# Optimization experiments

Measured on AMD Instinct MI355X. Metric: run time of the kernel, lower is better.

The kernel has to match this reference:

```python
import jax, jax.numpy as jnp
import numpy as np
from jax import lax

B, C_IN, C_OUT, N, R, K = 16, 64, 64, 32768, 32, 3
GROUPS, GN_EPS = 8, 1e-5


def swish(x):
    return x * jax.nn.sigmoid(x)


def group_norm(x, gamma, beta):
    b, c = x.shape[:2]
    xg = x.reshape(b, GROUPS, -1)
    mu = xg.mean(-1, keepdims=True)
    var = xg.var(-1, keepdims=True)
    xn = ((xg - mu) * lax.rsqrt(var + GN_EPS)).reshape(x.shape)
    shp = (1, c) + (1,) * (x.ndim - 2)
    return xn * gamma.reshape(shp) + beta.reshape(shp)


def conv3d(x, w, b):
    y = lax.conv_general_dilated(x, w, (1, 1, 1), 'SAME',
                                 dimension_numbers=('NCDHW', 'OIDHW', 'NCDHW'))
    return y + b.reshape(1, -1, 1, 1, 1)


def voxelize(features, coords):
    # features [B,C,N], coords [B,3,N] -> vox [B,C,R,R,R], norm_coords [B,3,N] in [0,R-1]
    c = coords - coords.mean(axis=2, keepdims=True)
    scale = jnp.linalg.norm(c, axis=1, keepdims=True).max(axis=2, keepdims=True) * 2.0  # eps=0
    norm = jnp.clip((c / scale + 0.5) * R, 0.0, R - 1)
    vc = jnp.round(norm).astype(jnp.int32)
    idx = (vc[:, 0] * R + vc[:, 1]) * R + vc[:, 2]  # [B,N] flat voxel index

    def per_batch(f, i):  # f [C,N], i [N] -> [C, R^3] scatter-average
        sums = jax.ops.segment_sum(f.T, i, num_segments=R ** 3)  # [R^3, C]
        cnt = jax.ops.segment_sum(jnp.ones(i.shape, f.dtype), i, num_segments=R ** 3)
        return (sums / jnp.maximum(cnt, 1.0)[:, None]).T

    vox = jax.vmap(per_batch)(features, idx).reshape(features.shape[0], features.shape[1], R, R, R)
    return vox, norm


def trilinear_devoxelize(vox, coords):
    # vox [B,C,R,R,R], coords [B,3,N] float in [0,R-1] -> [B,C,N]
    b, c = vox.shape[:2]
    flat = vox.reshape(b, c, R ** 3)
    c0f = jnp.floor(coords)
    f = coords - c0f
    i0 = jnp.clip(c0f.astype(jnp.int32), 0, R - 1)
    i1 = jnp.clip(i0 + 1, 0, R - 1)
    out = jnp.zeros((b, c, coords.shape[2]), vox.dtype)
    for xi, wx in ((i0[:, 0], 1.0 - f[:, 0]), (i1[:, 0], f[:, 0])):
        for yi, wy in ((i0[:, 1], 1.0 - f[:, 1]), (i1[:, 1], f[:, 1])):
            for zi, wz in ((i0[:, 2], 1.0 - f[:, 2]), (i1[:, 2], f[:, 2])):
                idx = (xi * R + yi) * R + zi  # [B,N]
                w = (wx * wy * wz)[:, None, :]
                out = out + jnp.take_along_axis(flat, idx[:, None, :], axis=2) * w
    return out


def setup_inputs():
    key = jax.random.key(0)
    ks = jax.random.split(key, 6)
    s1 = 1.0 / np.sqrt(C_IN * K ** 3)
    s2 = 1.0 / np.sqrt(C_OUT * K ** 3)
    sp = 1.0 / np.sqrt(C_IN)
    return {
        'features': jax.random.normal(ks[0], (B, C_IN, N), jnp.float32),
        'coords': jax.random.normal(ks[1], (B, 3, N), jnp.float32),
        'w1': jax.random.normal(ks[2], (C_OUT, C_IN, K, K, K), jnp.float32) * s1,
        'b1': jnp.zeros((C_OUT,), jnp.float32),
        'g1': jnp.ones((C_OUT,), jnp.float32),
        'be1': jnp.zeros((C_OUT,), jnp.float32),
        'w2': jax.random.normal(ks[3], (C_OUT, C_OUT, K, K, K), jnp.float32) * s2,
        'b2': jnp.zeros((C_OUT,), jnp.float32),
        'g2': jnp.ones((C_OUT,), jnp.float32),
        'be2': jnp.zeros((C_OUT,), jnp.float32),
        'wp': jax.random.normal(ks[4], (C_OUT, C_IN), jnp.float32) * sp,
        'bp': jnp.zeros((C_OUT,), jnp.float32),
        'gp': jnp.ones((C_OUT,), jnp.float32),
        'bep': jnp.zeros((C_OUT,), jnp.float32),
    }


def reference(features, coords, w1, b1, g1, be1, w2, b2, g2, be2, wp, bp, gp, bep):
    coords_sg = lax.stop_gradient(coords)  # torch: coords.detach() inside Voxelization
    vox, norm_coords = voxelize(features, coords_sg)
    h = swish(group_norm(conv3d(vox, w1, b1), g1, be1))
    # Dropout(0.1) is identity in eval mode
    h = swish(group_norm(conv3d(h, w2, b2), g2, be2))
    vpts = trilinear_devoxelize(h, norm_coords)
    pf = swish(group_norm(jnp.einsum('oc,bcn->bon', wp, features) + bp[None, :, None], gp, bep))
    return (vpts + pf, coords)
```

## Files before the change

kernel.cpp:

```cpp
#include <hip/hip_runtime.h>
#include <hip/hip_bf16.h>
#include <math.h>

#define BB   16
#define CCH  64
#define NPT  32768
#define RR   32
#define R3   32768
#define GSZ  262144
#define VOXB 2228224

typedef __attribute__((ext_vector_type(8))) short bfx8;
typedef __attribute__((ext_vector_type(8))) unsigned short usx8;
typedef __attribute__((ext_vector_type(16))) float f32x16;

__device__ __forceinline__ short f2bf(float f) {
    unsigned u = __builtin_bit_cast(unsigned, f);
    u += 0x7fff + ((u >> 16) & 1);
    return (short)(u >> 16);
}
__device__ __forceinline__ float bf2f(unsigned short s) {
    unsigned u = ((unsigned)s) << 16;
    return __builtin_bit_cast(float, u);
}

__device__ __forceinline__ float blockReduceSumF(float v) {
    __shared__ float sm[16];
    #pragma unroll
    for (int o = 32; o > 0; o >>= 1) v += __shfl_down(v, o);
    __syncthreads();
    if ((threadIdx.x & 63) == 0) sm[threadIdx.x >> 6] = v;
    __syncthreads();
    float s = 0.f;
    int nw = blockDim.x >> 6;
    for (int i = 0; i < nw; ++i) s += sm[i];
    return s;
}

__device__ __forceinline__ float blockReduceMaxF(float v) {
    __shared__ float sm[16];
    #pragma unroll
    for (int o = 32; o > 0; o >>= 1) v = fmaxf(v, __shfl_down(v, o));
    __syncthreads();
    if ((threadIdx.x & 63) == 0) sm[threadIdx.x >> 6] = v;
    __syncthreads();
    float s = sm[0];
    int nw = blockDim.x >> 6;
    for (int i = 1; i < nw; ++i) s = fmaxf(s, sm[i]);
    return s;
}

__global__ void k_cstat_sum(const float* __restrict__ coords, float* __restrict__ csum) {
    int b = blockIdx.x >> 3, seg = blockIdx.x & 7;
    const float* cb = coords + (size_t)b * 3 * NPT;
    int n0 = seg << 12;
    float sx = 0.f, sy = 0.f, sz = 0.f;
    for (int n = n0 + threadIdx.x; n < n0 + 4096; n += 256) {
        sx += cb[n]; sy += cb[NPT + n]; sz += cb[2 * NPT + n];
    }
    sx = blockReduceSumF(sx);
    sy = blockReduceSumF(sy);
    sz = blockReduceSumF(sz);
    if (threadIdx.x == 0) {
        atomicAdd(&csum[b * 4 + 0], sx);
        atomicAdd(&csum[b * 4 + 1], sy);
        atomicAdd(&csum[b * 4 + 2], sz);
    }
}

__global__ void k_cstat_max(const float* __restrict__ coords, const float* __restrict__ csum,
                            int* __restrict__ cmax) {
    int b = blockIdx.x >> 3, seg = blockIdx.x & 7;
    const float* cb = coords + (size_t)b * 3 * NPT;
    float mx = csum[b * 4 + 0] * (1.f / NPT);
    float my = csum[b * 4 + 1] * (1.f / NPT);
    float mz = csum[b * 4 + 2] * (1.f / NPT);
    int n0 = seg << 12;
    float mn = 0.f;
    for (int n = n0 + threadIdx.x; n < n0 + 4096; n += 256) {
        float x = cb[n] - mx, y = cb[NPT + n] - my, z = cb[2 * NPT + n] - mz;
        mn = fmaxf(mn, sqrtf(x * x + y * y + z * z));
    }
    mn = blockReduceMaxF(mn);
    if (threadIdx.x == 0) atomicMax(&cmax[b], __float_as_int(mn));
}

__global__ void k_norm_idx(const float* __restrict__ coords, const float* __restrict__ csum,
                           const int* __restrict__ cmax,
                           float* __restrict__ normc, int* __restrict__ vidx,
                           int* __restrict__ hist, float* __restrict__ out2) {
    int t = blockIdx.x * 256 + threadIdx.x;
    int b = t >> 15, n = t & 32767;
    float mx = csum[b * 4 + 0] * (1.f / NPT);
    float my = csum[b * 4 + 1] * (1.f / NPT);
    float mz = csum[b * 4 + 2] * (1.f / NPT);
    float scale = 2.f * __int_as_float(cmax[b]);
    const float* cb = coords + (size_t)b * 3 * NPT;
    float x = cb[n], y = cb[NPT + n], z = cb[2 * NPT + n];
    float nx = fminf(fmaxf(((x - mx) / scale + 0.5f) * 32.f, 0.f), 31.f);
    float ny = fminf(fmaxf(((y - my) / scale + 0.5f) * 32.f, 0.f), 31.f);
    float nz = fminf(fmaxf(((z - mz) / scale + 0.5f) * 32.f, 0.f), 31.f);
    float* nb = normc + (size_t)b * 3 * NPT;
    nb[n] = nx; nb[NPT + n] = ny; nb[2 * NPT + n] = nz;
    int vx = (int)rintf(nx), vy = (int)rintf(ny), vz = (int)rintf(nz);
    int v = (vx * 32 + vy) * 32 + vz;
    vidx[t] = v;
    atomicAdd(&hist[(b << 15) + v], 1);
    float* o2 = out2 + (size_t)b * 3 * NPT;
    o2[n] = x; o2[NPT + n] = y; o2[2 * NPT + n] = z;
}

__global__ __launch_bounds__(1024) void k_prefix(const int* __restrict__ hist,
                                                 int* __restrict__ startB,
                                                 int* __restrict__ base) {
    int b = blockIdx.x;
    int tid = threadIdx.x;
    const int* h = hist + (b << 15);
    int loc[32];
    int s = 0;
    #pragma unroll
    for (int j = 0; j < 32; ++j) { loc[j] = h[tid * 32 + j]; s += loc[j]; }
    __shared__ int sm[1024];
    sm[tid] = s;
    __syncthreads();
    for (int o = 1; o < 1024; o <<= 1) {
        int v = (tid >= o) ? sm[tid - o] : 0;
        __syncthreads();
        sm[tid] += v;
        __syncthreads();
    }
    int run = (tid ? sm[tid - 1] : 0);
    #pragma unroll
    for (int j = 0; j < 32; ++j) {
        int idx = (b << 15) + tid * 32 + j;
        startB[idx] = run;
        base[idx] = run;
        run += loc[j];
    }
}

__global__ __launch_bounds__(256) void k_reorder(const float* __restrict__ feat,
                                                 const int* __restrict__ vidx,
                                                 int* __restrict__ base,
                                                 short* __restrict__ featT) {
    __shared__ float tile[64][65];
    __shared__ int sslot[64];
    int blk = blockIdx.x;
    int b = blk >> 9;
    int n0 = (blk & 511) << 6;
    int tid = threadIdx.x;
    const float* fb = feat + ((size_t)b << 21);
    for (int e = tid; e < 64 * 64; e += 256) {
        int c = e >> 6, nn = e & 63;
        tile[c][nn] = fb[((size_t)c << 15) + n0 + nn];
    }
    if (tid < 64) {
        int v = vidx[(b << 15) + n0 + tid];
        sslot[tid] = atomicAdd(&base[(b << 15) + v], 1);
    }
    __syncthreads();
    int p = tid >> 2, q = tid & 3;
    int slot = sslot[p];
    short* dst = featT + (((size_t)((b << 15) + slot)) << 6) + q * 16;
    unsigned pk[8];
    #pragma unroll
    for (int k = 0; k < 8; ++k) {
        unsigned lo16 = (unsigned short)f2bf(tile[q * 16 + 2 * k][p]);
        unsigned hi16 = (unsigned short)f2bf(tile[q * 16 + 2 * k + 1][p]);
        pk[k] = lo16 | (hi16 << 16);
    }
    *(int4*)dst = make_int4(pk[0], pk[1], pk[2], pk[3]);
    *(int4*)(dst + 8) = make_int4(pk[4], pk[5], pk[6], pk[7]);
}

__global__ void k_vox_accum(const short* __restrict__ featT, const int* __restrict__ startB,
                            const int* __restrict__ base, short* __restrict__ vout) {
    int t = blockIdx.x * 256 + threadIdx.x;
    int lane4 = t & 15;
    int v = (t >> 4) & 32767;
    int b = t >> 19;
    int start = startB[(b << 15) + v];
    int end   = base[(b << 15) + v];
    float4 acc = make_float4(0.f, 0.f, 0.f, 0.f);
    const short* fT = featT + (((size_t)b << 15) << 6) + lane4 * 4;
    for (int p = start; p < end; ++p) {
        short4 hv = *(const short4*)(fT + ((size_t)p << 6));
        acc.x += bf2f((unsigned short)hv.x);
        acc.y += bf2f((unsigned short)hv.y);
        acc.z += bf2f((unsigned short)hv.z);
        acc.w += bf2f((unsigned short)hv.w);
    }
    float rc = 1.f / fmaxf((float)(end - start), 1.f);
    short4 pk;
    pk.x = f2bf(acc.x * rc); pk.y = f2bf(acc.y * rc);
    pk.z = f2bf(acc.z * rc); pk.w = f2bf(acc.w * rc);
    *(short4*)(vout + (size_t)b * VOXB + ((size_t)(v >> 5) * 34 + (v & 31) + 1) * 64 + lane4 * 4) = pk;
}

__global__ void k_wprep(const float* __restrict__ w, short* __restrict__ wT) {
    int e = blockIdx.x * 256 + threadIdx.x;
    int ci = e & 63, co = (e >> 6) & 63, k = e >> 12;
    wT[e] = f2bf(w[(size_t)(co * 64 + ci) * 27 + k]);
}

__global__ __launch_bounds__(256, 2) void k_conv_mfma(
    const short* __restrict__ vin, const short* __restrict__ wT,
    const float* __restrict__ bias, short* __restrict__ vout, float* __restrict__ st)
{
    __shared__ short lds[36 * 1088];
    __shared__ float sred[8][2];
    int bid = blockIdx.x;
    int xcd = bid & 7, sub = bid >> 3;
    int b = (xcd << 1) | (sub >> 6);
    int tile = sub & 63;
    int x0 = (tile >> 3) << 2, y0 = (tile & 7) << 2;
    int tid = threadIdx.x;
    int wv = tid >> 6, l = tid & 63;
    int lo = l & 31, hi = l >> 5;
    const short* vb = vin + (size_t)b * VOXB;
    int xo = x0 + wv;
    if (tid < 16) ((float*)sred)[tid] = 0.f;

    f32x16 acc[2][4];
    #pragma unroll
    for (int cb = 0; cb < 2; ++cb)
        #pragma unroll
        for (int j = 0; j < 4; ++j)
            #pragma unroll
            for (int i = 0; i < 16; ++i) acc[cb][j][i] = 0.f;

    #pragma unroll
    for (int h = 0; h < 2; ++h) {
        if (h) __syncthreads();
        for (int e = tid; e < 4896; e += 256) {
            int line = e / 136, r = e - line * 136;
            int z = r >> 2, q = r & 3;
            int xx = line / 6, yy = line - xx * 6;
            int xi = x0 + xx - 1, yi = y0 + yy - 1;
            int4 v = make_int4(0, 0, 0, 0);
            if ((unsigned)xi < 32u && (unsigned)yi < 32u)
                v = *(const int4*)(vb + ((size_t)(xi * 32 + yi) * 34 + z) * 64 + h * 32 + q * 8);
            int dst = line * 1088 + z * 32 + ((q * 8) ^ ((z & 3) << 3));
            *(int4*)(lds + dst) = v;
        }
        __syncthreads();
        const short* whb = wT + h * 32 + lo * 64 + hi * 8;
        #pragma unroll
        for (int dx = 0; dx < 3; ++dx) {
            #pragma unroll
            for (int dy = 0; dy < 3; ++dy) {
                const short* lbase = lds + ((wv + dx) * 6 + dy) * 1088;
                #pragma unroll
                for (int dz = 0; dz < 3; ++dz) {
                    const int tap = dx * 9 + dy * 3 + dz;
                    const short* wt = whb + tap * 4096;
                    bfx8 a0 = *(const bfx8*)(wt);
                    bfx8 a1 = *(const bfx8*)(wt + 2048);
                    bfx8 a2 = *(const bfx8*)(wt + 16);
                    bfx8 a3 = *(const bfx8*)(wt + 2048 + 16);
                    int zz = dz + lo;
                    int so = (zz & 3) << 3;
                    int s0 = (hi * 8) ^ so;
                    int s1 = (16 + hi * 8) ^ so;
                    const short* bb0 = lbase + zz * 32;
                    #pragma unroll
                    for (int j = 0; j < 4; ++j) {
                        const short* bp = bb0 + j * 1088;
                        bfx8 b0 = *(const bfx8*)(bp + s0);
                        bfx8 b1 = *(const bfx8*)(bp + s1);
                        acc[0][j] = __builtin_amdgcn_mfma_f32_32x32x16_bf16(a0, b0, acc[0][j], 0, 0, 0);
                        acc[1][j] = __builtin_amdgcn_mfma_f32_32x32x16_bf16(a1, b0, acc[1][j], 0, 0, 0);
                        acc[0][j] = __builtin_amdgcn_mfma_f32_32x32x16_bf16(a2, b1, acc[0][j], 0, 0, 0);
                        acc[1][j] = __builtin_amdgcn_mfma_f32_32x32x16_bf16(a3, b1, acc[1][j], 0, 0, 0);
                    }
                }
            }
        }
    }

    float gs[8], gs2[8];
    #pragma unroll
    for (int g = 0; g < 8; ++g) { gs[g] = 0.f; gs2[g] = 0.f; }
    short* ob = vout + (size_t)b * VOXB;
    #pragma unroll
    for (int cb = 0; cb < 2; ++cb) {
        #pragma unroll
        for (int j = 0; j < 4; ++j) {
            size_t rb = ((size_t)(xo * 32 + y0 + j) * 34 + 1 + lo) * 64;
            #pragma unroll
            for (int q = 0; q < 4; ++q) {
                int co0 = cb * 32 + hi * 4 + q * 8;
                float v0 = acc[cb][j][q * 4 + 0] + bias[co0 + 0];
                float v1 = acc[cb][j][q * 4 + 1] + bias[co0 + 1];
                float v2 = acc[cb][j][q * 4 + 2] + bias[co0 + 2];
                float v3 = acc[cb][j][q * 4 + 3] + bias[co0 + 3];
                int g = cb * 4 + q;
                gs[g] += v0 + v1 + v2 + v3;
                gs2[g] += v0 * v0 + v1 * v1 + v2 * v2 + v3 * v3;
                short4 pk;
                pk.x = f2bf(v0); pk.y = f2bf(v1); pk.z = f2bf(v2); pk.w = f2bf(v3);
                *(short4*)(ob + rb + co0) = pk;
            }
        }
    }
    #pragma unroll
    for (int g = 0; g < 8; ++g) {
        float s = gs[g], s2 = gs2[g];
        #pragma unroll
        for (int o = 32; o > 0; o >>= 1) { s += __shfl_down(s, o); s2 += __shfl_down(s2, o); }
        if (l == 0) { atomicAdd(&sred[g][0], s); atomicAdd(&sred[g][1], s2); }
    }
    __syncthreads();
    if (tid < 8) {
        atomicAdd(&st[((b << 3) + tid) * 2 + 0], sred[tid][0]);
        atomicAdd(&st[((b << 3) + tid) * 2 + 1], sred[tid][1]);
    }
}

__global__ void k_gn_apply_b(short* __restrict__ v, const float* __restrict__ st,
                             const float* __restrict__ gamma, const float* __restrict__ beta) {
    int e = blockIdx.x * 256 + threadIdx.x;
    int cg = e & 7, vx = (e >> 3) & 32767, b = e >> 18;
    float s = st[(b * 8 + cg) * 2 + 0], s2 = st[(b * 8 + cg) * 2 + 1];
    float mean = s * (1.f / 262144.f);
    float var = s2 * (1.f / 262144.f) - mean * mean;
    float rstd = rsqrtf(var + 1e-5f);
    short* p = v + (size_t)b * VOXB + ((size_t)(vx >> 5) * 34 + (vx & 31) + 1) * 64 + cg * 8;
    usx8 hv = *(const usx8*)p;
    usx8 ov;
    #pragma unroll
    for (int i = 0; i < 8; ++i) {
        int co = cg * 8 + i;
        float f = bf2f(hv[i]);
        float g = (f - mean) * rstd * gamma[co] + beta[co];
        float sw = g / (1.f + __expf(-g));
        ov[i] = (unsigned short)f2bf(sw);
    }
    *(usx8*)p = ov;
}

__global__ __launch_bounds__(256) void k_point(const float* __restrict__ feat,
                                               const float* __restrict__ wp,
                                               const float* __restrict__ bp,
                                               short* __restrict__ pbuf,
                                               float* __restrict__ stp) {
    __shared__ float s_f[64][64];
    __shared__ float s_w[64][68];
    __shared__ float sred[8][2];
    int nblk = blockIdx.x * 64;
    int b = blockIdx.y;
    int tid = threadIdx.x;
    if (tid < 16) ((float*)sred)[tid] = 0.f;
    const float* fb = feat + (((size_t)b * CCH) << 15);
    for (int e = tid; e < 64 * 64; e += 256) {
        int c = e >> 6, nn = e & 63;
        s_f[c][nn] = fb[(((size_t)c) << 15) + nblk + nn];
        s_w[nn][c] = wp[e];
    }
    __syncthreads();
    int o0 = (tid >> 4) << 2;
    int n0 = (tid & 15) << 2;
    float acc[4][4] = {{0.f}};
    for (int c = 0; c < 64; ++c) {
        float4 fv = *(const float4*)&s_f[c][n0];
        float4 wv = *(const float4*)&s_w[c][o0];
        float fvv[4] = {fv.x, fv.y, fv.z, fv.w};
        float wvv[4] = {wv.x, wv.y, wv.z, wv.w};
        #pragma unroll
        for (int j = 0; j < 4; ++j)
            #pragma unroll
            for (int i = 0; i < 4; ++i) acc[j][i] += wvv[j] * fvv[i];
    }
    float s = 0.f, s2 = 0.f;
    #pragma unroll
    for (int j = 0; j < 4; ++j) {
        float bb = bp[o0 + j];
        short* op = pbuf + (((size_t)(b * CCH + o0 + j)) << 15) + nblk + n0;
        short4 pk;
        float v0 = acc[j][0] + bb, v1 = acc[j][1] + bb;
        float v2 = acc[j][2] + bb, v3 = acc[j][3] + bb;
        s += v0 + v1 + v2 + v3;
        s2 += v0 * v0 + v1 * v1 + v2 * v2 + v3 * v3;
        pk.x = f2bf(v0); pk.y = f2bf(v1); pk.z = f2bf(v2); pk.w = f2bf(v3);
        *(short4*)op = pk;
    }
    int g = o0 >> 3;
    atomicAdd(&sred[g][0], s);
    atomicAdd(&sred[g][1], s2);
    __syncthreads();
    if (tid < 8) {
        atomicAdd(&stp[(b * 8 + tid) * 2 + 0], sred[tid][0]);
        atomicAdd(&stp[(b * 8 + tid) * 2 + 1], sred[tid][1]);
    }
}

__global__ void k_final(const short* __restrict__ h, const float* __restrict__ normc,
                        const float* __restrict__ stp, const float* __restrict__ gp,
                        const float* __restrict__ bep, const short* __restrict__ pbuf,
                        float* __restrict__ out1) {
    int tid = threadIdx.x;
    int s = tid & 7, pp = tid >> 3;
    int pt = blockIdx.x * 32 + pp;
    int b = pt >> 15, n = pt & 32767;
    const float* nb = normc + (size_t)b * 3 * NPT;
    float nx = nb[n], ny = nb[NPT + n], nz = nb[2 * NPT + n];
    float fxf = floorf(nx), fyf = floorf(ny), fzf = floorf(nz);
    float fx = nx - fxf, fy = ny - fyf, fz = nz - fzf;
    int x0 = (int)fxf; x0 = x0 < 31 ? x0 : 31;
    int y0 = (int)fyf; y0 = y0 < 31 ? y0 : 31;
    int z0 = (int)fzf; z0 = z0 < 31 ? z0 : 31;
    int x1 = x0 + 1 < 31 ? x0 + 1 : 31;
    int y1 = y0 + 1 < 31 ? y0 + 1 : 31;
    int z1 = z0 + 1 < 31 ? z0 + 1 : 31;
    float wx0 = 1.f - fx, wx1 = fx, wy0 = 1.f - fy, wy1 = fy, wz0 = 1.f - fz, wz1 = fz;
    const short* hb = h + (size_t)b * VOXB + s * 8;
    float acc[8];
    #pragma unroll
    for (int i = 0; i < 8; ++i) acc[i] = 0.f;
    #pragma unroll
    for (int cx = 0; cx < 2; ++cx) {
        int xi = cx ? x1 : x0; float wxx = cx ? wx1 : wx0;
        #pragma unroll
        for (int cy = 0; cy < 2; ++cy) {
            int yi = cy ? y1 : y0; float wyy = cy ? wy1 : wy0;
            #pragma unroll
            for (int cz = 0; cz < 2; ++cz) {
                int zi = cz ? z1 : z0; float wzz = cz ? wz1 : wz0;
                float w = wxx * wyy * wzz;
                usx8 hv = *(const usx8*)(hb + ((size_t)(xi * 32 + yi) * 34 + zi + 1) * 64);
                #pragma unroll
                for (int i = 0; i < 8; ++i) acc[i] = fmaf(w, bf2f(hv[i]), acc[i]);
            }
        }
    }
    float ss = stp[(b * 8 + s) * 2 + 0], ss2 = stp[(b * 8 + s) * 2 + 1];
    float mean = ss * (1.f / 262144.f);
    float rstd = rsqrtf(ss2 * (1.f / 262144.f) - mean * mean + 1e-5f);
    const short* pb = pbuf + (((size_t)(b * CCH)) << 15) + n;
    #pragma unroll
    for (int i = 0; i < 8; ++i) {
        int co = s * 8 + i;
        float* op = out1 + (((size_t)(b * CCH + co)) << 15) + n;
        float pv = bf2f((unsigned short)pb[((size_t)co) << 15]);
        float g = (pv - mean) * rstd * gp[co] + bep[co];
        float sw = g / (1.f + __expf(-g));
        *op = acc[i] + sw;
    }
}

extern "C" void kernel_launch(void* const* d_in, const int* in_sizes, int n_in,
                              void* d_out, int out_size, void* d_ws, size_t ws_size,
                              hipStream_t stream) {
    const float* feat   = (const float*)d_in[0];
    const float* coords = (const float*)d_in[1];
    const float* w1  = (const float*)d_in[2];
    const float* b1  = (const float*)d_in[3];
    const float* g1  = (const float*)d_in[4];
    const float* be1 = (const float*)d_in[5];
    const float* w2  = (const float*)d_in[6];
    const float* b2  = (const float*)d_in[7];
    const float* g2  = (const float*)d_in[8];
    const float* be2 = (const float*)d_in[9];
    const float* wp  = (const float*)d_in[10];
    const float* bp  = (const float*)d_in[11];
    const float* gp  = (const float*)d_in[12];
    const float* bep = (const float*)d_in[13];

    float* out1 = (float*)d_out;
    float* out2 = out1 + (size_t)BB * CCH * NPT;

    const size_t reg0Bytes = (size_t)BB * NPT * CCH * 4;
    short* featT    = (short*)d_ws;
    short* voxT_mid = (short*)d_ws;
    short* pbuf     = (short*)d_ws;
    short* voxT_in  = (short*)((char*)d_ws + reg0Bytes);
    char* p = (char*)voxT_in + (size_t)BB * VOXB * 2;
    int*   hist   = (int*)p;  p += (size_t)BB * R3 * 4;
    int*   startB = (int*)p;  p += (size_t)BB * R3 * 4;
    int*   base   = (int*)p;  p += (size_t)BB * R3 * 4;
    float* normc = (float*)p; p += (size_t)BB * 3 * NPT * 4;
    int*   vidx  = (int*)p;   p += (size_t)BB * NPT * 4;
    short* wT1   = (short*)p; p += 110592 * 2;
    short* wT2   = (short*)p; p += 110592 * 2;
    float* st1   = (float*)p; p += 256 * 4;
    float* st2   = (float*)p; p += 256 * 4;
    float* stp   = (float*)p; p += 256 * 4;
    float* csum  = (float*)p; p += 64 * 4;
    int*   cmax  = (int*)p;   p += 16 * 4;

    hipMemsetAsync(voxT_in, 0, (size_t)BB * VOXB * 2, stream);
    hipMemsetAsync(hist, 0, (size_t)BB * R3 * 4, stream);
    hipMemsetAsync(st1, 0, (256 * 3 + 64 + 16) * 4, stream);

    k_cstat_sum<<<128, 256, 0, stream>>>(coords, csum);
    k_cstat_max<<<128, 256, 0, stream>>>(coords, csum, cmax);
    k_norm_idx<<<(BB * NPT) / 256, 256, 0, stream>>>(coords, csum, cmax, normc, vidx, hist, out2);
    k_prefix<<<BB, 1024, 0, stream>>>(hist, startB, base);
    k_reorder<<<(BB * NPT) / 64, 256, 0, stream>>>(feat, vidx, base, featT);
    k_vox_accum<<<(BB * R3 * 16) / 256, 256, 0, stream>>>(featT, startB, base, voxT_in);
    k_wprep<<<432, 256, 0, stream>>>(w1, wT1);
    k_wprep<<<432, 256, 0, stream>>>(w2, wT2);

    hipMemsetAsync(voxT_mid, 0, (size_t)BB * VOXB * 2, stream);

    k_conv_mfma<<<1024, 256, 0, stream>>>(voxT_in, wT1, b1, voxT_mid, st1);
    k_gn_apply_b<<<(BB * R3 * 8) / 256, 256, 0, stream>>>(voxT_mid, st1, g1, be1);

    k_conv_mfma<<<1024, 256, 0, stream>>>(voxT_mid, wT2, b2, voxT_in, st2);
    k_gn_apply_b<<<(BB * R3 * 8) / 256, 256, 0, stream>>>(voxT_in, st2, g2, be2);

    k_point<<<dim3(NPT / 64, BB), 256, 0, stream>>>(feat, wp, bp, pbuf, stp);

    k_final<<<(BB * NPT) / 32, 256, 0, stream>>>(voxT_in, normc, stp, gp, bep, pbuf, out1);
}
```

Before: 757.3 us.

## Reuse LDS B-fragments across dy taps and zero only padding slices

The conv inner loop is restructured so each LDS row vector is loaded once and applied to up to three dy taps, with the weights for all three dy held in registers. This cuts LDS reads per MFMA from one per tap to roughly six per three taps, at the cost of more weight registers. The full-buffer memsets of the padded voxel grids are replaced by a small kernel that zeroes only the z=0 and z=33 padding planes, on the assumption that every interior voxel is written by accumulation or by the conv.

```diff
diff --git a/kernel.cpp b/kernel.cpp
--- a/kernel.cpp
+++ b/kernel.cpp
@@ -197,6 +197,13 @@
     *(short4*)(vout + (size_t)b * VOXB + ((size_t)(v >> 5) * 34 + (v & 31) + 1) * 64 + lane4 * 4) = pk;
 }
 
+__global__ void k_padzero(short* __restrict__ v) {
+    int t = blockIdx.x * 256 + threadIdx.x;
+    int q = t & 7, zp = (t >> 3) & 1, xy = (t >> 4) & 1023, b = t >> 14;
+    int z = zp ? 33 : 0;
+    *(int4*)(v + (size_t)b * VOXB + ((size_t)xy * 34 + z) * 64 + q * 8) = make_int4(0, 0, 0, 0);
+}
+
 __global__ void k_wprep(const float* __restrict__ w, short* __restrict__ wT) {
     int e = blockIdx.x * 256 + threadIdx.x;
     int ci = e & 63, co = (e >> 6) & 63, k = e >> 12;
@@ -244,34 +251,40 @@
             *(int4*)(lds + dst) = v;
         }
         __syncthreads();
-        const short* whb = wT + h * 32 + lo * 64 + hi * 8;
+        const short* wbase = wT + lo * 64 + h * 32 + hi * 8;
         #pragma unroll
         for (int dx = 0; dx < 3; ++dx) {
+            const short* ldsx = lds + ((wv + dx) * 6) * 1088;
             #pragma unroll
-            for (int dy = 0; dy < 3; ++dy) {
-                const short* lbase = lds + ((wv + dx) * 6 + dy) * 1088;
+            for (int dz = 0; dz < 3; ++dz) {
+                int zz = lo + dz;
+                int swz = (zz & 3) << 3;
+                const short* bcol = ldsx + zz * 32;
                 #pragma unroll
-                for (int dz = 0; dz < 3; ++dz) {
-                    const int tap = dx * 9 + dy * 3 + dz;
-                    const short* wt = whb + tap * 4096;
-                    bfx8 a0 = *(const bfx8*)(wt);
-                    bfx8 a1 = *(const bfx8*)(wt + 2048);
-                    bfx8 a2 = *(const bfx8*)(wt + 16);
-                    bfx8 a3 = *(const bfx8*)(wt + 2048 + 16);
-                    int zz = dz + lo;
-                    int so = (zz & 3) << 3;
-                    int s0 = (hi * 8) ^ so;
-                    int s1 = (16 + hi * 8) ^ so;
-                    const short* bb0 = lbase + zz * 32;
+                for (int s = 0; s < 2; ++s) {
+                    int slot = (s * 16 + hi * 8) ^ swz;
+                    const short* wt0 = wbase + (dx * 9 + dz) * 4096 + s * 16;
+                    bfx8 wA0 = *(const bfx8*)(wt0);
+                    bfx8 wB0 = *(const bfx8*)(wt0 + 2048);
+                    bfx8 wA1 = *(const bfx8*)(wt0 + 3 * 4096);
+                    bfx8 wB1 = *(const bfx8*)(wt0 + 3 * 4096 + 2048);
+                    bfx8 wA2 = *(const bfx8*)(wt0 + 6 * 4096);
+                    bfx8 wB2 = *(const bfx8*)(wt0 + 6 * 4096 + 2048);
                     #pragma unroll
-                    for (int j = 0; j < 4; ++j) {
-                        const short* bp = bb0 + j * 1088;
-                        bfx8 b0 = *(const bfx8*)(bp + s0);
-                        bfx8 b1 = *(const bfx8*)(bp + s1);
-                        acc[0][j] = __builtin_amdgcn_mfma_f32_32x32x16_bf16(a0, b0, acc[0][j], 0, 0, 0);
-                        acc[1][j] = __builtin_amdgcn_mfma_f32_32x32x16_bf16(a1, b0, acc[1][j], 0, 0, 0);
-                        acc[0][j] = __builtin_amdgcn_mfma_f32_32x32x16_bf16(a2, b1, acc[0][j], 0, 0, 0);
-                        acc[1][j] = __builtin_amdgcn_mfma_f32_32x32x16_bf16(a3, b1, acc[1][j], 0, 0, 0);
+                    for (int L = 0; L < 6; ++L) {
+                        bfx8 bv = *(const bfx8*)(bcol + L * 1088 + slot);
+                        if (L <= 3) {
+                            acc[0][L] = __builtin_amdgcn_mfma_f32_32x32x16_bf16(wA0, bv, acc[0][L], 0, 0, 0);
+                            acc[1][L] = __builtin_amdgcn_mfma_f32_32x32x16_bf16(wB0, bv, acc[1][L], 0, 0, 0);
+                        }
+                        if (L >= 1 && L <= 4) {
+                            acc[0][L-1] = __builtin_amdgcn_mfma_f32_32x32x16_bf16(wA1, bv, acc[0][L-1], 0, 0, 0);
+                            acc[1][L-1] = __builtin_amdgcn_mfma_f32_32x32x16_bf16(wB1, bv, acc[1][L-1], 0, 0, 0);
+                        }
+                        if (L >= 2) {
+                            acc[0][L-2] = __builtin_amdgcn_mfma_f32_32x32x16_bf16(wA2, bv, acc[0][L-2], 0, 0, 0);
+                            acc[1][L-2] = __builtin_amdgcn_mfma_f32_32x32x16_bf16(wB2, bv, acc[1][L-2], 0, 0, 0);
+                        }
                     }
                 }
             }
@@ -488,10 +501,10 @@
     float* csum  = (float*)p; p += 64 * 4;
     int*   cmax  = (int*)p;   p += 16 * 4;
 
-    hipMemsetAsync(voxT_in, 0, (size_t)BB * VOXB * 2, stream);
     hipMemsetAsync(hist, 0, (size_t)BB * R3 * 4, stream);
     hipMemsetAsync(st1, 0, (256 * 3 + 64 + 16) * 4, stream);
 
+    k_padzero<<<1024, 256, 0, stream>>>(voxT_in);
     k_cstat_sum<<<128, 256, 0, stream>>>(coords, csum);
     k_cstat_max<<<128, 256, 0, stream>>>(coords, csum, cmax);
     k_norm_idx<<<(BB * NPT) / 256, 256, 0, stream>>>(coords, csum, cmax, normc, vidx, hist, out2);
@@ -501,7 +514,7 @@
     k_wprep<<<432, 256, 0, stream>>>(w1, wT1);
     k_wprep<<<432, 256, 0, stream>>>(w2, wT2);
 
-    hipMemsetAsync(voxT_mid, 0, (size_t)BB * VOXB * 2, stream);
+    k_padzero<<<1024, 256, 0, stream>>>(voxT_mid);
 
     k_conv_mfma<<<1024, 256, 0, stream>>>(voxT_in, wT1, b1, voxT_mid, st1);
     k_gn_apply_b<<<(BB * R3 * 8) / 256, 256, 0, stream>>>(voxT_mid, st1, g1, be1);
```

After: 745.1 us. No clear change (-1.6%).
